# Kernel optimization log

Measured on AMD Instinct MI355X. Metric: run time of the kernel, lower is better.

## Reference

```python
import jax, jax.numpy as jnp
import numpy as np

N = 50000      # nodes
E = 800000     # edges
FIN = 128      # num_feature
EDIM = 16      # edge_dim
OUT = 64       # out_dim (per-head channels; concat=False averages heads)
H = 4          # heads
SCALE = 1.0 / float(np.sqrt(OUT))


def _layernorm(h, g, b):
    mu = h.mean(-1, keepdims=True)
    var = ((h - mu) ** 2).mean(-1, keepdims=True)
    return (h - mu) * jax.lax.rsqrt(var + 1e-5) * g + b


def _tconv(x, src, dst, ea, Wq, bq, Wk, bk, Wv, bv, We, Ws, bs):
    # PyG TransformerConv, concat=False, root_weight=True, eval mode (no dropout)
    n = x.shape[0]
    q = (x @ Wq + bq).reshape(n, H, OUT)[dst]   # [E,H,D] query at destination
    k = (x @ Wk + bk).reshape(n, H, OUT)[src]   # [E,H,D] key at source
    v = (x @ Wv + bv).reshape(n, H, OUT)[src]   # [E,H,D] value at source
    e = (ea @ We).reshape(-1, H, OUT)           # [E,H,D] edge embedding (no bias)
    logits = jnp.einsum('ehd,ehd->eh', q, k + e) * SCALE   # [E,H]
    # segment softmax over incoming edges of each destination node
    m = jax.lax.stop_gradient(jax.ops.segment_max(logits, dst, num_segments=n))
    a = jnp.exp(logits - m[dst])
    s = jax.ops.segment_sum(a, dst, num_segments=n)
    alpha = a / s[dst]                                     # [E,H]
    agg = jax.ops.segment_sum((v + e) * alpha[..., None], dst, num_segments=n)  # [N,H,D]
    return agg.mean(axis=1) + x @ Ws + bs      # concat=False -> head mean; + skip


def _forward(x, src, dst, ea, p1, p2, p3, g, b):
    h = x
    for p in (p1, p2, p3):
        h = jax.nn.gelu(_layernorm(_tconv(h, src, dst, ea, *p), g, b), approximate=False)
    return h


def setup_inputs() -> dict:
    key = jax.random.key(0)
    ks = iter(jax.random.split(key, 64))
    def nrm(shp, s=0.05):
        return jax.random.normal(next(ks), shp, jnp.float32) * s
    inp = {
        'x': nrm((N, FIN), 1.0),
        'edge_index': jax.random.randint(next(ks), (2, E), 0, N),
        'edge_attr': nrm((E, EDIM), 1.0),
    }
    for l, fin in ((1, FIN), (2, OUT), (3, OUT)):
        inp[f'Wq{l}'] = nrm((fin, H * OUT)); inp[f'bq{l}'] = jnp.zeros((H * OUT,), jnp.float32)
        inp[f'Wk{l}'] = nrm((fin, H * OUT)); inp[f'bk{l}'] = jnp.zeros((H * OUT,), jnp.float32)
        inp[f'Wv{l}'] = nrm((fin, H * OUT)); inp[f'bv{l}'] = jnp.zeros((H * OUT,), jnp.float32)
        inp[f'We{l}'] = nrm((EDIM, H * OUT))
        inp[f'Ws{l}'] = nrm((fin, OUT)); inp[f'bs{l}'] = jnp.zeros((OUT,), jnp.float32)
    inp['ln_g'] = jnp.ones((OUT,), jnp.float32)
    inp['ln_b'] = jnp.zeros((OUT,), jnp.float32)
    return inp


def reference(x, edge_index, edge_attr,
              Wq1, bq1, Wk1, bk1, Wv1, bv1, We1, Ws1, bs1,
              Wq2, bq2, Wk2, bk2, Wv2, bv2, We2, Ws2, bs2,
              Wq3, bq3, Wk3, bk3, Wv3, bv3, We3, Ws3, bs3,
              ln_g, ln_b):
    src, dst = edge_index[0], edge_index[1]
    p1 = (Wq1, bq1, Wk1, bk1, Wv1, bv1, We1, Ws1, bs1)
    p2 = (Wq2, bq2, Wk2, bk2, Wv2, bv2, We2, Ws2, bs2)
    p3 = (Wq3, bq3, Wk3, bk3, Wv3, bv3, We3, Ws3, bs3)
    return _forward(x, src, dst, edge_attr, p1, p2, p3, ln_g, ln_b)
```

## Files before the change

kernel.cpp:

```cpp
#include <hip/hip_runtime.h>
#include <hip/hip_bf16.h>
#include <math.h>

#define NNODES 50000
#define NEDGES 800000
#define HD     256
#define CW     384
#define NTOT   896
#define QS     0.18033688011112042f

typedef __hip_bfloat16 bf16;
typedef unsigned short u16;
typedef unsigned char  u8;
typedef unsigned int   u32;
typedef unsigned long long u64;
typedef __attribute__((ext_vector_type(8))) short bf16x8;
typedef __attribute__((ext_vector_type(4))) float f32x4;
typedef __attribute__((ext_vector_type(2))) float f32x2;

__device__ __forceinline__ float lo16f(u32 u) { return __uint_as_float(u << 16); }
__device__ __forceinline__ float hi16f(u32 u) { return __uint_as_float(u & 0xFFFF0000u); }
__device__ __forceinline__ short f2s(float v) { __hip_bfloat16 h = __float2bfloat16(v); return *(short*)&h; }

template<int CTRL>
__device__ __forceinline__ float dppadd(float x) {
    int t = __builtin_amdgcn_update_dpp(0, __float_as_int(x), CTRL, 0xF, 0xF, true);
    return x + __int_as_float(t);
}

__global__ void hist_kernel(const int* __restrict__ dst, int* __restrict__ deg, int E) {
    int e = blockIdx.x * 256 + threadIdx.x;
    if (e < E) atomicAdd(&deg[dst[e]], 1);
}

__global__ void scanA(const int* __restrict__ deg, int* __restrict__ locincl,
                      int* __restrict__ blocksum, int n) {
    int tid = threadIdx.x;
    int i = blockIdx.x * 256 + tid;
    int v = (i < n) ? deg[i] : 0;
    int lane = tid & 63, w = tid >> 6;
    int s = v;
    #pragma unroll
    for (int off = 1; off < 64; off <<= 1) {
        int t = __shfl_up(s, off);
        if (lane >= off) s += t;
    }
    __shared__ int wsum[4];
    if (lane == 63) wsum[w] = s;
    __syncthreads();
    for (int ww = 0; ww < w; ww++) s += wsum[ww];
    if (i < n) locincl[i] = s;
    if (tid == 255) blocksum[blockIdx.x] = s;
}

__global__ void scanB(const int* __restrict__ blocksum, int* __restrict__ blockoff,
                      int nb, int* __restrict__ rowptr, int n) {
    int tid = threadIdx.x;
    int v = (tid < nb) ? blocksum[tid] : 0;
    int lane = tid & 63, w = tid >> 6;
    int s = v;
    #pragma unroll
    for (int off = 1; off < 64; off <<= 1) {
        int t = __shfl_up(s, off);
        if (lane >= off) s += t;
    }
    __shared__ int wsum[4];
    if (lane == 63) wsum[w] = s;
    __syncthreads();
    for (int ww = 0; ww < w; ww++) s += wsum[ww];
    if (tid < nb) blockoff[tid] = s - v;
    if (tid == 255) rowptr[n] = s;
}

__global__ void scanC(const int* __restrict__ deg, const int* __restrict__ locincl,
                      const int* __restrict__ blockoff,
                      int* __restrict__ rowptr, int* __restrict__ cursor, int n) {
    int i = blockIdx.x * 256 + threadIdx.x;
    if (i < n) {
        int ex = locincl[i] - deg[i] + blockoff[blockIdx.x];
        rowptr[i] = ex;
        cursor[i] = ex;
    }
}

__global__ void scatter_kernel(const int* __restrict__ src, const int* __restrict__ dst,
                               int* __restrict__ cursor, int2* __restrict__ csr2, int E) {
    int e = blockIdx.x * 256 + threadIdx.x;
    if (e < E) {
        int d = dst[e];
        int p = atomicAdd(&cursor[d], 1);
        csr2[p] = make_int2(src[e], e);
    }
}

__global__ void pack_all(const float* __restrict__ Wq, const float* __restrict__ bq,
                         const float* __restrict__ Wk, const float* __restrict__ bk,
                         const float* __restrict__ Wv, const float* __restrict__ bv,
                         const float* __restrict__ We,
                         const float* __restrict__ Ws, const float* __restrict__ bs,
                         bf16* __restrict__ Wc, float* __restrict__ b, int K) {
    int n = blockIdx.x, c = threadIdx.x;
    float v, bb;
    if (n < 256)      { v = Wq[(size_t)c * 256 + n] * QS;    bb = bq[n] * QS; }
    else if (n < 320) {
        int t = n - 256, h = t >> 4, j = t & 15;
        float s = 0.f, sb = 0.f;
        #pragma unroll 8
        for (int d = 0; d < 64; d++) {
            float wv = We[j * HD + h * 64 + d];
            s += Wq[(size_t)c * 256 + h * 64 + d] * wv;
            sb += bq[h * 64 + d] * wv;
        }
        v = s * QS; bb = sb * QS;
    }
    else if (n < 384) { v = Ws[(size_t)c * 64  + (n - 320)]; bb = bs[n - 320]; }
    else if (n < 640) { v = Wv[(size_t)c * 256 + (n - 384)]; bb = bv[n - 384]; }
    else              { v = Wk[(size_t)c * 256 + (n - 640)]; bb = bk[n - 640]; }
    Wc[(size_t)n * K + c] = __float2bfloat16(v);
    if (c == 0) b[n] = bb;
}

template<typename TA, int K>
__global__ void __launch_bounds__(256) gemm_lds(
    const TA* __restrict__ A, const bf16* __restrict__ Wc, const float* __restrict__ bias,
    bf16* __restrict__ comb, bf16* __restrict__ vbuf, u8* __restrict__ k8)
{
    constexpr int KS  = K / 32;
    constexpr int CPR = K / 8;
    constexpr int ITERS = 4;
    __shared__ short Bl[128 * K];
    int tid = threadIdx.x, w = tid >> 6, lane = tid & 63;
    int cl = lane & 15, aq = lane >> 4;
    int c0 = blockIdx.x * 2;

    #pragma unroll
    for (int p = 0; p < CPR / 2; p++) {
        int slot = tid + p * 256;
        int row = slot / CPR, j = slot % CPR;
        *(uint4*)&Bl[row * K + ((j ^ (row & 7)) << 3)] =
            *(const uint4*)((const u16*)Wc + (size_t)(c0 * 64 + row) * K + (j << 3));
    }
    __syncthreads();

    int mrow = blockIdx.y * (64 * ITERS) + w * 16 + cl;

    auto LOADA = [&](bf16x8* af, int m) {
        int rc = (m < NNODES) ? m : (NNODES - 1);
        if constexpr (sizeof(TA) == 4) {
            const float* ar = (const float*)A + (size_t)rc * K + aq * 8;
            #pragma unroll
            for (int ks = 0; ks < KS; ks++) {
                const float4* ap = (const float4*)(ar + ks * 32);
                float4 f0 = ap[0], f1 = ap[1];
                union { short s[8]; bf16x8 v; } t;
                t.s[0] = f2s(f0.x); t.s[1] = f2s(f0.y); t.s[2] = f2s(f0.z); t.s[3] = f2s(f0.w);
                t.s[4] = f2s(f1.x); t.s[5] = f2s(f1.y); t.s[6] = f2s(f1.z); t.s[7] = f2s(f1.w);
                af[ks] = t.v;
            }
        } else {
            const u16* ar = (const u16*)A + (size_t)rc * K + aq * 8;
            #pragma unroll
            for (int ks = 0; ks < KS; ks++) af[ks] = *(const bf16x8*)(ar + ks * 32);
        }
    };

    bf16x8 cur[KS], nxt[KS];
    LOADA(cur, mrow);
    #pragma unroll
    for (int it = 0; it < ITERS; it++) {
        int m = mrow + it * 64;
        if (it + 1 < ITERS) LOADA(nxt, m + 64);
        #pragma unroll
        for (int c = 0; c < 2; c++) {
            int chunk = c0 + c;
            f32x4 acc[4] = {};
            #pragma unroll
            for (int t = 0; t < 4; t++) {
                #pragma unroll
                for (int ks = 0; ks < KS; ks++) {
                    bf16x8 bfr = *(const bf16x8*)&Bl[(c * 64 + t * 16 + cl) * K +
                                                     (((ks * 4 + aq) ^ (cl & 7)) << 3)];
                    acc[t] = __builtin_amdgcn_mfma_f32_16x16x32_bf16(bfr, cur[ks], acc[t], 0, 0, 0);
                }
            }
            if (m < NNODES) {
                if (chunk < 10) {
                    u16* dst = (chunk < 6) ? (u16*)comb + (size_t)m * CW + chunk * 64
                                           : (u16*)vbuf + (size_t)m * 256 + (chunk - 6) * 64;
                    #pragma unroll
                    for (int t = 0; t < 4; t++) {
                        float4 bv = *(const float4*)&bias[chunk * 64 + t * 16 + aq * 4];
                        u32 lo = (u32)(u16)f2s(acc[t][0] + bv.x) | ((u32)(u16)f2s(acc[t][1] + bv.y) << 16);
                        u32 hi = (u32)(u16)f2s(acc[t][2] + bv.z) | ((u32)(u16)f2s(acc[t][3] + bv.w) << 16);
                        *(uint2*)(dst + t * 16 + aq * 4) = make_uint2(lo, hi);
                    }
                } else {
                    u8* dst = k8 + (size_t)m * 256 + (chunk - 10) * 64;
                    #pragma unroll
                    for (int t = 0; t < 4; t++) {
                        float4 bv = *(const float4*)&bias[chunk * 64 + t * 16 + aq * 4];
                        u32 pk = __builtin_amdgcn_cvt_pk_fp8_f32(acc[t][0] + bv.x, acc[t][1] + bv.y, 0, false);
                        pk = __builtin_amdgcn_cvt_pk_fp8_f32(acc[t][2] + bv.z, acc[t][3] + bv.w, pk, true);
                        *(u32*)(dst + t * 16 + aq * 4) = pk;
                    }
                }
            }
        }
        #pragma unroll
        for (int ks = 0; ks < KS; ks++) cur[ks] = nxt[ks];
    }
}

__global__ void __launch_bounds__(256) node_fused(
    const int* __restrict__ rowptr, const int2* __restrict__ csr2,
    const float* __restrict__ eattr, const u16* __restrict__ comb,
    const u16* __restrict__ vbuf, const u8* __restrict__ k8,
    const float* __restrict__ We, const float* __restrict__ lng, const float* __restrict__ lnb,
    bf16* __restrict__ outB, float* __restrict__ outF)
{
    int tid = threadIdx.x, w = tid >> 6, lane = tid & 63;
    int n = blockIdx.x * 4 + w;
    int hg = lane >> 4, j16 = lane & 15, coff = 4 * lane;
    __shared__ float sAV[4][256];
    __shared__ float sAE[4][64];

    const u16* crow = comb + (size_t)n * CW;
    uint2 qv = *(const uint2*)(crow + coff);
    float qf0 = lo16f(qv.x), qf1 = hi16f(qv.x), qf2 = lo16f(qv.y), qf3 = hi16f(qv.y);
    float qwe_r = __uint_as_float((u32)crow[256 + lane] << 16);

    int e0 = __builtin_amdgcn_readfirstlane(rowptr[n]);
    int e1 = __builtin_amdgcn_readfirstlane(rowptr[n + 1]);

    float ss = 0.f, av0 = 0.f, av1 = 0.f, av2 = 0.f, av3 = 0.f, ae = 0.f;
    u32 vo = (u32)coff * 2u;
    u32 eo = (u32)j16 * 4u;

    auto EDGE = [&](int2 me) {
        u32 s   = (u32)__builtin_amdgcn_readfirstlane(me.x);
        u32 eid = (u32)__builtin_amdgcn_readfirstlane(me.y);
        const char* kp = (const char*)k8    + ((size_t)s << 8);
        const char* vp = (const char*)vbuf  + ((size_t)s << 9);
        const char* ep = (const char*)eattr + ((size_t)eid << 6);
        u32   kw = *(const u32*)  (kp + coff);
        uint2 vw = *(const uint2*)(vp + vo);
        float ea = *(const float*)(ep + eo);
        f32x2 k01 = __builtin_amdgcn_cvt_pk_f32_fp8(kw, false);
        f32x2 k23 = __builtin_amdgcn_cvt_pk_f32_fp8(kw, true);
        float part = qf0 * k01[0] + qf1 * k01[1] + qf2 * k23[0] + qf3 * k23[1] + qwe_r * ea;
        part = dppadd<0xB1>(part);
        part = dppadd<0x4E>(part);
        part = dppadd<0x141>(part);
        part = dppadd<0x140>(part);
        float alpha = __builtin_amdgcn_exp2f(part);
        ss += alpha;
        ae += alpha * ea;
        av0 += alpha * lo16f(vw.x); av1 += alpha * hi16f(vw.x);
        av2 += alpha * lo16f(vw.y); av3 += alpha * hi16f(vw.y);
    };

    int i = e0;
    int2 c0 = make_int2(0, 0), c1 = c0, c2 = c0, c3 = c0;
    if (i + 3 < e1) { c0 = csr2[i]; c1 = csr2[i + 1]; c2 = csr2[i + 2]; c3 = csr2[i + 3]; }
    for (; i + 7 < e1; i += 4) {
        int2 p0 = csr2[i + 4], p1 = csr2[i + 5], p2 = csr2[i + 6], p3 = csr2[i + 7];
        EDGE(c0); EDGE(c1); EDGE(c2); EDGE(c3);
        c0 = p0; c1 = p1; c2 = p2; c3 = p3;
    }
    if (i + 3 < e1) { EDGE(c0); EDGE(c1); EDGE(c2); EDGE(c3); i += 4; }
    for (; i < e1; ++i) { int2 cc = csr2[i]; EDGE(cc); }

    float inv = (ss > 0.f) ? 1.f / ss : 0.f;
    *(float4*)&sAV[w][coff] = make_float4(av0 * inv, av1 * inv, av2 * inv, av3 * inv);
    sAE[w][lane] = ae * inv;

    int d = lane;
    float val = 0.f;
    #pragma unroll
    for (int h = 0; h < 4; h++) {
        float xv = sAV[w][h * 64 + d];
        #pragma unroll
        for (int j = 0; j < 16; j++) xv += sAE[w][h * 16 + j] * We[j * HD + h * 64 + d];
        val += xv;
    }
    val = val * 0.25f + __uint_as_float((u32)crow[320 + d] << 16);

    float m = val;
    #pragma unroll
    for (int off = 1; off < 64; off <<= 1) m += __shfl_xor(m, off);
    m *= (1.f / 64.f);
    float diff = val - m;
    float vr = diff * diff;
    #pragma unroll
    for (int off = 1; off < 64; off <<= 1) vr += __shfl_xor(vr, off);
    vr *= (1.f / 64.f);
    float y = diff * rsqrtf(vr + 1e-5f) * lng[d] + lnb[d];
    float ge = 0.5f * y * (1.f + erff(y * 0.70710678118654752f));
    if (outF) outF[(size_t)n * 64 + d] = ge;
    else      outB[(size_t)n * 64 + d] = __float2bfloat16(ge);
}

extern "C" void kernel_launch(void* const* d_in, const int* in_sizes, int n_in,
                              void* d_out, int out_size, void* d_ws, size_t ws_size,
                              hipStream_t stream)
{
    const float* x     = (const float*)d_in[0];
    const int*   eidx  = (const int*)d_in[1];
    const float* eattr = (const float*)d_in[2];
    struct P { const float *Wq,*bq,*Wk,*bk,*Wv,*bv,*We,*Ws,*bs; };
    P p[3];
    for (int l = 0; l < 3; l++) {
        int base = 3 + l * 9;
        p[l].Wq = (const float*)d_in[base + 0]; p[l].bq = (const float*)d_in[base + 1];
        p[l].Wk = (const float*)d_in[base + 2]; p[l].bk = (const float*)d_in[base + 3];
        p[l].Wv = (const float*)d_in[base + 4]; p[l].bv = (const float*)d_in[base + 5];
        p[l].We = (const float*)d_in[base + 6];
        p[l].Ws = (const float*)d_in[base + 7]; p[l].bs = (const float*)d_in[base + 8];
    }
    const float* lng = (const float*)d_in[30];
    const float* lnb = (const float*)d_in[31];

    char* ws = (char*)d_ws;
    size_t off = 0;
    auto alloc = [&](size_t bytes) { void* pp = ws + off; off += (bytes + 255) & ~(size_t)255; return pp; };
    int*   rowptr   = (int*)  alloc((NNODES + 1) * 4);
    int*   cursor   = (int*)  alloc(NNODES * 4);
    int*   deg      = (int*)  alloc(NNODES * 4);
    int*   blocksum = (int*)  alloc(256 * 4);
    int*   blockoff = (int*)  alloc(256 * 4);
    int2*  csr2     = (int2*) alloc((size_t)NEDGES * 8);
    bf16*  hbuf     = (bf16*) alloc((size_t)NNODES * 64 * 2);
    bf16*  comb     = (bf16*) alloc((size_t)NNODES * CW * 2);
    bf16*  vbuf     = (bf16*) alloc((size_t)NNODES * 256 * 2);
    u8*    k8       = (u8*)   alloc((size_t)NNODES * 256);
    bf16*  Wc       = (bf16*) alloc((size_t)NTOT * 128 * 2);
    float* b896     = (float*)alloc(NTOT * 4);
    (void)ws_size;

    const int* srcArr = eidx;
    const int* dstArr = eidx + NEDGES;

    int NB = (NNODES + 255) / 256;
    (void)hipMemsetAsync(deg, 0, NNODES * 4, stream);
    hist_kernel<<<(NEDGES + 255) / 256, 256, 0, stream>>>(dstArr, deg, NEDGES);
    scanA<<<NB, 256, 0, stream>>>(deg, cursor, blocksum, NNODES);
    scanB<<<1, 256, 0, stream>>>(blocksum, blockoff, NB, rowptr, NNODES);
    scanC<<<NB, 256, 0, stream>>>(deg, cursor, blockoff, rowptr, cursor, NNODES);
    scatter_kernel<<<(NEDGES + 255) / 256, 256, 0, stream>>>(srcArr, dstArr, cursor, csr2, NEDGES);

    int NBY = (NNODES + 255) / 256;
    int fins[3] = {128, 64, 64};

    const void* hin = x;
    for (int l = 0; l < 3; l++) {
        int FIN = fins[l];
        pack_all<<<NTOT, FIN, 0, stream>>>(p[l].Wq, p[l].bq, p[l].Wk, p[l].bk,
                                           p[l].Wv, p[l].bv, p[l].We, p[l].Ws, p[l].bs,
                                           Wc, b896, FIN);
        if (l == 0) gemm_lds<float, 128><<<dim3(7, NBY), 256, 0, stream>>>((const float*)hin, Wc, b896, comb, vbuf, k8);
        else        gemm_lds<bf16,  64><<<dim3(7, NBY), 256, 0, stream>>>((const bf16*)hin,  Wc, b896, comb, vbuf, k8);
        node_fused<<<NNODES / 4, 256, 0, stream>>>(rowptr, csr2, eattr, (const u16*)comb,
            (const u16*)vbuf, k8, p[l].We, lng, lnb,
            (l == 2) ? nullptr : hbuf, (l == 2) ? (float*)d_out : nullptr);
        hin = hbuf;
    }
}
```

Baseline: 689.9 us.

## Split node edge loop across two waves, register-resident GEMM weights, pre-cast x

The node kernel now assigns two wavefronts per destination node. Each wave processes half of the incoming edges, and the partial softmax sums and aggregates are combined through shared memory before LayerNorm/GELU, which targets latency in the gather-bound edge loop. The GEMM drops its LDS weight staging and instead holds one 64-column weight chunk per block in registers, with more row iterations per block. A separate cast kernel converts x to bf16 up front. The trade-offs are a block barrier, idle half-waves in the epilogue, higher register pressure in the GEMM, and an extra pass over x.

```diff
diff --git a/kernel.cpp b/kernel.cpp
--- a/kernel.cpp
+++ b/kernel.cpp
@@ -13,7 +13,6 @@
 typedef unsigned short u16;
 typedef unsigned char  u8;
 typedef unsigned int   u32;
-typedef unsigned long long u64;
 typedef __attribute__((ext_vector_type(8))) short bf16x8;
 typedef __attribute__((ext_vector_type(4))) float f32x4;
 typedef __attribute__((ext_vector_type(2))) float f32x2;
@@ -91,6 +90,16 @@
         int p = atomicAdd(&cursor[d], 1);
         csr2[p] = make_int2(src[e], e);
     }
+}
+
+__global__ void xcast(const float* __restrict__ x, u16* __restrict__ xb) {
+    int i = blockIdx.x * 256 + threadIdx.x;
+    const float4* p = (const float4*)(x + (size_t)i * 8);
+    float4 a = p[0], b = p[1];
+    union { u16 s[8]; uint4 u; } t;
+    t.s[0] = (u16)f2s(a.x); t.s[1] = (u16)f2s(a.y); t.s[2] = (u16)f2s(a.z); t.s[3] = (u16)f2s(a.w);
+    t.s[4] = (u16)f2s(b.x); t.s[5] = (u16)f2s(b.y); t.s[6] = (u16)f2s(b.z); t.s[7] = (u16)f2s(b.w);
+    *(uint4*)(xb + (size_t)i * 8) = t.u;
 }
 
 __global__ void pack_all(const float* __restrict__ Wq, const float* __restrict__ bq,
@@ -120,48 +129,35 @@
     if (c == 0) b[n] = bb;
 }
 
-template<typename TA, int K>
-__global__ void __launch_bounds__(256) gemm_lds(
-    const TA* __restrict__ A, const bf16* __restrict__ Wc, const float* __restrict__ bias,
+template<int K>
+__global__ void __launch_bounds__(256) gemm_reg(
+    const u16* __restrict__ A, const bf16* __restrict__ Wc, const float* __restrict__ bias,
     bf16* __restrict__ comb, bf16* __restrict__ vbuf, u8* __restrict__ k8)
 {
-    constexpr int KS  = K / 32;
-    constexpr int CPR = K / 8;
-    constexpr int ITERS = 4;
-    __shared__ short Bl[128 * K];
+    constexpr int KS = K / 32;
+    constexpr int ITERS = 8;
     int tid = threadIdx.x, w = tid >> 6, lane = tid & 63;
     int cl = lane & 15, aq = lane >> 4;
-    int c0 = blockIdx.x * 2;
-
-    #pragma unroll
-    for (int p = 0; p < CPR / 2; p++) {
-        int slot = tid + p * 256;
-        int row = slot / CPR, j = slot % CPR;
-        *(uint4*)&Bl[row * K + ((j ^ (row & 7)) << 3)] =
-            *(const uint4*)((const u16*)Wc + (size_t)(c0 * 64 + row) * K + (j << 3));
-    }
-    __syncthreads();
-
+    int chunk = blockIdx.x;
     int mrow = blockIdx.y * (64 * ITERS) + w * 16 + cl;
+
+    bf16x8 bfr[4][KS];
+    #pragma unroll
+    for (int t = 0; t < 4; t++)
+        #pragma unroll
+        for (int ks = 0; ks < KS; ks++)
+            bfr[t][ks] = *(const bf16x8*)((const u16*)Wc +
+                         (size_t)(chunk * 64 + t * 16 + cl) * K + ks * 32 + aq * 8);
+
+    float4 bv[4];
+    #pragma unroll
+    for (int t = 0; t < 4; t++) bv[t] = *(const float4*)&bias[chunk * 64 + t * 16 + aq * 4];
 
     auto LOADA = [&](bf16x8* af, int m) {
         int rc = (m < NNODES) ? m : (NNODES - 1);
-        if constexpr (sizeof(TA) == 4) {
-            const float* ar = (const float*)A + (size_t)rc * K + aq * 8;
-            #pragma unroll
-            for (int ks = 0; ks < KS; ks++) {
-                const float4* ap = (const float4*)(ar + ks * 32);
-                float4 f0 = ap[0], f1 = ap[1];
-                union { short s[8]; bf16x8 v; } t;
-                t.s[0] = f2s(f0.x); t.s[1] = f2s(f0.y); t.s[2] = f2s(f0.z); t.s[3] = f2s(f0.w);
-                t.s[4] = f2s(f1.x); t.s[5] = f2s(f1.y); t.s[6] = f2s(f1.z); t.s[7] = f2s(f1.w);
-                af[ks] = t.v;
-            }
-        } else {
-            const u16* ar = (const u16*)A + (size_t)rc * K + aq * 8;
-            #pragma unroll
-            for (int ks = 0; ks < KS; ks++) af[ks] = *(const bf16x8*)(ar + ks * 32);
-        }
+        const u16* ar = A + (size_t)rc * K + aq * 8;
+        #pragma unroll
+        for (int ks = 0; ks < KS; ks++) af[ks] = *(const bf16x8*)(ar + ks * 32);
     };
 
     bf16x8 cur[KS], nxt[KS];
@@ -170,39 +166,30 @@
     for (int it = 0; it < ITERS; it++) {
         int m = mrow + it * 64;
         if (it + 1 < ITERS) LOADA(nxt, m + 64);
-        #pragma unroll
-        for (int c = 0; c < 2; c++) {
-            int chunk = c0 + c;
-            f32x4 acc[4] = {};
+        f32x4 acc[4] = {};
+        #pragma unroll
+        for (int t = 0; t < 4; t++)
             #pragma unroll
-            for (int t = 0; t < 4; t++) {
+            for (int ks = 0; ks < KS; ks++)
+                acc[t] = __builtin_amdgcn_mfma_f32_16x16x32_bf16(bfr[t][ks], cur[ks], acc[t], 0, 0, 0);
+
+        if (m < NNODES) {
+            if (chunk < 10) {
+                u16* dst = (chunk < 6) ? (u16*)comb + (size_t)m * CW + chunk * 64
+                                       : (u16*)vbuf + (size_t)m * 256 + (chunk - 6) * 64;
                 #pragma unroll
-                for (int ks = 0; ks < KS; ks++) {
-                    bf16x8 bfr = *(const bf16x8*)&Bl[(c * 64 + t * 16 + cl) * K +
-                                                     (((ks * 4 + aq) ^ (cl & 7)) << 3)];
-                    acc[t] = __builtin_amdgcn_mfma_f32_16x16x32_bf16(bfr, cur[ks], acc[t], 0, 0, 0);
+                for (int t = 0; t < 4; t++) {
+                    u32 lo = (u32)(u16)f2s(acc[t][0] + bv[t].x) | ((u32)(u16)f2s(acc[t][1] + bv[t].y) << 16);
+                    u32 hi = (u32)(u16)f2s(acc[t][2] + bv[t].z) | ((u32)(u16)f2s(acc[t][3] + bv[t].w) << 16);
+                    *(uint2*)(dst + t * 16 + aq * 4) = make_uint2(lo, hi);
                 }
-            }
-            if (m < NNODES) {
-                if (chunk < 10) {
-                    u16* dst = (chunk < 6) ? (u16*)comb + (size_t)m * CW + chunk * 64
-                                           : (u16*)vbuf + (size_t)m * 256 + (chunk - 6) * 64;
-                    #pragma unroll
-                    for (int t = 0; t < 4; t++) {
-                        float4 bv = *(const float4*)&bias[chunk * 64 + t * 16 + aq * 4];
-                        u32 lo = (u32)(u16)f2s(acc[t][0] + bv.x) | ((u32)(u16)f2s(acc[t][1] + bv.y) << 16);
-                        u32 hi = (u32)(u16)f2s(acc[t][2] + bv.z) | ((u32)(u16)f2s(acc[t][3] + bv.w) << 16);
-                        *(uint2*)(dst + t * 16 + aq * 4) = make_uint2(lo, hi);
-                    }
-                } else {
-                    u8* dst = k8 + (size_t)m * 256 + (chunk - 10) * 64;
-                    #pragma unroll
-                    for (int t = 0; t < 4; t++) {
-                        float4 bv = *(const float4*)&bias[chunk * 64 + t * 16 + aq * 4];
-                        u32 pk = __builtin_amdgcn_cvt_pk_fp8_f32(acc[t][0] + bv.x, acc[t][1] + bv.y, 0, false);
-                        pk = __builtin_amdgcn_cvt_pk_fp8_f32(acc[t][2] + bv.z, acc[t][3] + bv.w, pk, true);
-                        *(u32*)(dst + t * 16 + aq * 4) = pk;
-                    }
+            } else {
+                u8* dst = k8 + (size_t)m * 256 + (chunk - 10) * 64;
+                #pragma unroll
+                for (int t = 0; t < 4; t++) {
+                    u32 pk = __builtin_amdgcn_cvt_pk_fp8_f32(acc[t][0] + bv[t].x, acc[t][1] + bv[t].y, 0, false);
+                    pk = __builtin_amdgcn_cvt_pk_fp8_f32(acc[t][2] + bv[t].z, acc[t][3] + bv[t].w, pk, true);
+                    *(u32*)(dst + t * 16 + aq * 4) = pk;
                 }
             }
         }
@@ -219,10 +206,12 @@
     bf16* __restrict__ outB, float* __restrict__ outF)
 {
     int tid = threadIdx.x, w = tid >> 6, lane = tid & 63;
-    int n = blockIdx.x * 4 + w;
+    int n = blockIdx.x * 2 + (w >> 1);
+    int half = w & 1;
     int hg = lane >> 4, j16 = lane & 15, coff = 4 * lane;
     __shared__ float sAV[4][256];
     __shared__ float sAE[4][64];
+    __shared__ float sSS[4][4];
 
     const u16* crow = comb + (size_t)n * CW;
     uint2 qv = *(const uint2*)(crow + coff);
@@ -231,6 +220,9 @@
 
     int e0 = __builtin_amdgcn_readfirstlane(rowptr[n]);
     int e1 = __builtin_amdgcn_readfirstlane(rowptr[n + 1]);
+    int mid = e0 + ((e1 - e0 + 1) >> 1);
+    int lo = half ? mid : e0;
+    int hi = half ? e1 : mid;
 
     float ss = 0.f, av0 = 0.f, av1 = 0.f, av2 = 0.f, av3 = 0.f, ae = 0.f;
     u32 vo = (u32)coff * 2u;
@@ -259,45 +251,59 @@
         av2 += alpha * lo16f(vw.y); av3 += alpha * hi16f(vw.y);
     };
 
-    int i = e0;
+    int i = lo;
     int2 c0 = make_int2(0, 0), c1 = c0, c2 = c0, c3 = c0;
-    if (i + 3 < e1) { c0 = csr2[i]; c1 = csr2[i + 1]; c2 = csr2[i + 2]; c3 = csr2[i + 3]; }
-    for (; i + 7 < e1; i += 4) {
+    if (i + 3 < hi) { c0 = csr2[i]; c1 = csr2[i + 1]; c2 = csr2[i + 2]; c3 = csr2[i + 3]; }
+    for (; i + 7 < hi; i += 4) {
         int2 p0 = csr2[i + 4], p1 = csr2[i + 5], p2 = csr2[i + 6], p3 = csr2[i + 7];
         EDGE(c0); EDGE(c1); EDGE(c2); EDGE(c3);
         c0 = p0; c1 = p1; c2 = p2; c3 = p3;
     }
-    if (i + 3 < e1) { EDGE(c0); EDGE(c1); EDGE(c2); EDGE(c3); i += 4; }
-    for (; i < e1; ++i) { int2 cc = csr2[i]; EDGE(cc); }
-
-    float inv = (ss > 0.f) ? 1.f / ss : 0.f;
-    *(float4*)&sAV[w][coff] = make_float4(av0 * inv, av1 * inv, av2 * inv, av3 * inv);
-    sAE[w][lane] = ae * inv;
-
-    int d = lane;
-    float val = 0.f;
-    #pragma unroll
-    for (int h = 0; h < 4; h++) {
-        float xv = sAV[w][h * 64 + d];
-        #pragma unroll
-        for (int j = 0; j < 16; j++) xv += sAE[w][h * 16 + j] * We[j * HD + h * 64 + d];
-        val += xv;
-    }
-    val = val * 0.25f + __uint_as_float((u32)crow[320 + d] << 16);
-
-    float m = val;
-    #pragma unroll
-    for (int off = 1; off < 64; off <<= 1) m += __shfl_xor(m, off);
-    m *= (1.f / 64.f);
-    float diff = val - m;
-    float vr = diff * diff;
-    #pragma unroll
-    for (int off = 1; off < 64; off <<= 1) vr += __shfl_xor(vr, off);
-    vr *= (1.f / 64.f);
-    float y = diff * rsqrtf(vr + 1e-5f) * lng[d] + lnb[d];
-    float ge = 0.5f * y * (1.f + erff(y * 0.70710678118654752f));
-    if (outF) outF[(size_t)n * 64 + d] = ge;
-    else      outB[(size_t)n * 64 + d] = __float2bfloat16(ge);
+    if (i + 3 < hi) { EDGE(c0); EDGE(c1); EDGE(c2); EDGE(c3); i += 4; }
+    for (; i < hi; ++i) { int2 cc = csr2[i]; EDGE(cc); }
+
+    *(float4*)&sAV[w][coff] = make_float4(av0, av1, av2, av3);
+    sAE[w][lane] = ae;
+    if (j16 == 0) sSS[w][hg] = ss;
+    __syncthreads();
+
+    if ((w & 1) == 0) {
+        float inv[4];
+        #pragma unroll
+        for (int h = 0; h < 4; h++) {
+            float S = sSS[w][h] + sSS[w + 1][h];
+            inv[h] = (S > 0.f) ? 1.f / S : 0.f;
+        }
+        {
+            float aet = (sAE[w][lane] + sAE[w + 1][lane]) * inv[hg];
+            sAE[w][lane] = aet;
+        }
+        int d = lane;
+        float val = 0.f;
+        #pragma unroll
+        for (int h = 0; h < 4; h++) {
+            float AV = sAV[w][h * 64 + d] + sAV[w + 1][h * 64 + d];
+            float xv = AV * inv[h];
+            #pragma unroll
+            for (int j = 0; j < 16; j++) xv += sAE[w][h * 16 + j] * We[j * HD + h * 64 + d];
+            val += xv;
+        }
+        val = val * 0.25f + __uint_as_float((u32)crow[320 + d] << 16);
+
+        float m = val;
+        #pragma unroll
+        for (int off = 1; off < 64; off <<= 1) m += __shfl_xor(m, off);
+        m *= (1.f / 64.f);
+        float diff = val - m;
+        float vr = diff * diff;
+        #pragma unroll
+        for (int off = 1; off < 64; off <<= 1) vr += __shfl_xor(vr, off);
+        vr *= (1.f / 64.f);
+        float y = diff * rsqrtf(vr + 1e-5f) * lng[d] + lnb[d];
+        float ge = 0.5f * y * (1.f + erff(y * 0.70710678118654752f));
+        if (outF) outF[(size_t)n * 64 + d] = ge;
+        else      outB[(size_t)n * 64 + d] = __float2bfloat16(ge);
+    }
 }
 
 extern "C" void kernel_launch(void* const* d_in, const int* in_sizes, int n_in,
@@ -330,6 +336,7 @@
     int*   blockoff = (int*)  alloc(256 * 4);
     int2*  csr2     = (int2*) alloc((size_t)NEDGES * 8);
     bf16*  hbuf     = (bf16*) alloc((size_t)NNODES * 64 * 2);
+    u16*   xb       = (u16*)  alloc((size_t)NNODES * 128 * 2);
     bf16*  comb     = (bf16*) alloc((size_t)NNODES * CW * 2);
     bf16*  vbuf     = (bf16*) alloc((size_t)NNODES * 256 * 2);
     u8*    k8       = (u8*)   alloc((size_t)NNODES * 256);
@@ -347,21 +354,22 @@
     scanB<<<1, 256, 0, stream>>>(blocksum, blockoff, NB, rowptr, NNODES);
     scanC<<<NB, 256, 0, stream>>>(deg, cursor, blockoff, rowptr, cursor, NNODES);
     scatter_kernel<<<(NEDGES + 255) / 256, 256, 0, stream>>>(srcArr, dstArr, cursor, csr2, NEDGES);
-
-    int NBY = (NNODES + 255) / 256;
+    xcast<<<(NNODES * 128 / 8 + 255) / 256, 256, 0, stream>>>(x, xb);
+
+    int NBY = (NNODES + 511) / 512;
     int fins[3] = {128, 64, 64};
 
-    const void* hin = x;
+    const u16* hin = xb;
     for (int l = 0; l < 3; l++) {
         int FIN = fins[l];
         pack_all<<<NTOT, FIN, 0, stream>>>(p[l].Wq, p[l].bq, p[l].Wk, p[l].bk,
                                            p[l].Wv, p[l].bv, p[l].We, p[l].Ws, p[l].bs,
                                            Wc, b896, FIN);
-        if (l == 0) gemm_lds<float, 128><<<dim3(7, NBY), 256, 0, stream>>>((const float*)hin, Wc, b896, comb, vbuf, k8);
-        else        gemm_lds<bf16,  64><<<dim3(7, NBY), 256, 0, stream>>>((const bf16*)hin,  Wc, b896, comb, vbuf, k8);
-        node_fused<<<NNODES / 4, 256, 0, stream>>>(rowptr, csr2, eattr, (const u16*)comb,
+        if (l == 0) gemm_reg<128><<<dim3(14, NBY), 256, 0, stream>>>(hin, Wc, b896, comb, vbuf, k8);
+        else        gemm_reg<64> <<<dim3(14, NBY), 256, 0, stream>>>(hin, Wc, b896, comb, vbuf, k8);
+        node_fused<<<NNODES / 2, 256, 0, stream>>>(rowptr, csr2, eattr, (const u16*)comb,
             (const u16*)vbuf, k8, p[l].We, lng, lnb,
             (l == 2) ? nullptr : hbuf, (l == 2) ? (float*)d_out : nullptr);
-        hin = hbuf;
-    }
-}
+        hin = (const u16*)hbuf;
+    }
+}
```

New measurement: 763.8 us. 10.7% more time.
